# Performance work log

Measured on AMD Instinct MI355X. Metric: run time of the kernel, lower is better.

Reference implementation:

```python
import jax, jax.numpy as jnp
import numpy as np

D_MODEL = 1024
N_HEAD = 16
N_BR = 4
DH = D_MODEL // N_HEAD            # 64
H_TOT = N_BR * N_HEAD             # 64
SCALE = float(np.pi / np.sqrt(3.0))
ATTN_SCALE = DH ** -0.5


def _rope(x):
    # x: (B, H, T, Dh). Non-interleaved variant: output is cat of the two rotated halves.
    B, H, T, Dh = x.shape
    inv_freq = 1.0 / (10000.0 ** (jnp.arange(0, Dh, 2, dtype=jnp.float32) / Dh))  # (Dh/2,)
    t = jnp.arange(T, dtype=jnp.float32)
    freqs = t[:, None] * inv_freq[None, :]        # (T, Dh/2)
    cos = jnp.cos(freqs)[None, None]              # (1,1,T,Dh/2)
    sin = jnp.sin(freqs)[None, None]
    x1 = x[..., 0::2]
    x2 = x[..., 1::2]
    return jnp.concatenate([-x2 * sin + x1 * cos, x1 * sin + x2 * cos], axis=-1)


def setup_inputs() -> dict:
    key = jax.random.key(0)
    ks = jax.random.split(key, 8)
    s = 0.02
    B, T = 1, 1024
    return {
        "X": jax.random.normal(ks[0], (B, T, D_MODEL), jnp.float32),
        "Wq": jax.random.normal(ks[1], (D_MODEL, H_TOT * DH), jnp.float32) * s,
        "bq": jnp.zeros((H_TOT * DH,), jnp.float32),
        "Wk": jax.random.normal(ks[2], (D_MODEL, D_MODEL), jnp.float32) * s,
        "bk": jnp.zeros((D_MODEL,), jnp.float32),
        "Wv": jax.random.normal(ks[3], (D_MODEL, H_TOT * DH), jnp.float32) * s,
        "bv": jnp.zeros((H_TOT * DH,), jnp.float32),
        "sink_scalars": jax.random.normal(ks[4], (H_TOT, 1, 1), jnp.float32) * s,
        "v_nulls": jax.random.normal(ks[5], (H_TOT, DH), jnp.float32) * s,
        "Wo": jax.random.normal(ks[6], (D_MODEL, D_MODEL), jnp.float32) * s,
        "bo": jnp.zeros((D_MODEL,), jnp.float32),
    }


def reference(X, Wq, bq, Wk, bk, Wv, bv, sink_scalars, v_nulls, Wo, bo):
    B, T, C = X.shape
    q = (X @ Wq + bq).reshape(B, T, H_TOT, DH).transpose(0, 2, 1, 3)   # (B,H,T,Dh)
    v = (X @ Wv + bv).reshape(B, T, H_TOT, DH).transpose(0, 2, 1, 3)
    k_base = (X @ Wk + bk).reshape(B, T, N_HEAD, DH).transpose(0, 2, 1, 3)  # (B,Nh,T,Dh)
    k = jnp.tile(k_base, (1, N_BR, 1, 1))                               # (B,H,T,Dh)

    q = _rope(q)
    k = _rope(k)

    scores = jnp.einsum('bhtd,bhsd->bhts', q, k) * ATTN_SCALE           # (B,H,T,T)
    key_self = jnp.clip(jnp.sum(k * k, axis=-1), 1e-6, None)            # (B,H,T)
    denom = jnp.sqrt(key_self)[:, :, None, :]                           # (B,H,1,T)
    w = jax.nn.softplus(scores / denom)

    causal = jnp.tril(jnp.ones((T, T), dtype=bool))                     # keep lower triangle
    w = jnp.where(causal[None, None], w, 0.0)
    w = w * jax.nn.sigmoid(SCALE * w)

    sinks = jnp.tanh(sink_scalars).reshape(1, H_TOT, 1, 1) + 1e-6       # (1,H,1,1)
    alpha = 1.0 / (jnp.sum(w, axis=-1, keepdims=True) + sinks + 1e-6)   # (B,H,T,1)
    probs_tokens = w * alpha
    probs_sink = sinks * alpha                                          # (B,H,T,1)

    out_tokens = jnp.einsum('bhts,bhsd->bhtd', probs_tokens, v)
    out_sinks = probs_sink * v_nulls[None, :, None, :]                  # (B,H,T,Dh)
    context = out_tokens + out_sinks                                    # (B,H,T,Dh)

    context = context.reshape(B, N_BR, N_HEAD, T, DH)
    context = context.transpose(0, 1, 3, 2, 4).reshape(B, N_BR, T, C)
    y = context @ Wo + bo                                               # (B,N_BR,T,C)
    return jnp.mean(y, axis=1)


if __name__ == "__main__":
    out = reference(**setup_inputs())
    print(out.shape)
```

## Files before the change

### kernel.cpp

```cpp
#include <hip/hip_runtime.h>
#include <math.h>

#define SILU_SCALE 1.8137993642342178f
#define QKV_N 9216
#define LN2 0.6931471805599453f
#define DNSCALE 0.18033688011112042f

typedef __attribute__((ext_vector_type(8))) short bf16x8;
typedef __attribute__((ext_vector_type(4))) float f32x4;

#if __has_builtin(__builtin_amdgcn_exp2f)
#define EXP2(x) __builtin_amdgcn_exp2f(x)
#else
#define EXP2(x) exp2f(x)
#endif
#if __has_builtin(__builtin_amdgcn_logf)
#define LOG2(x) __builtin_amdgcn_logf(x)
#else
#define LOG2(x) __log2f(x)
#endif

__device__ __forceinline__ unsigned short f2bf(float f){
    union { float f; unsigned int i; } u; u.f = f;
    unsigned int r = u.i + 0x7FFFu + ((u.i >> 16) & 1u);
    return (unsigned short)(r >> 16);
}
__device__ __forceinline__ float bf2f(unsigned short s){
    union { unsigned int i; float f; } u; u.i = ((unsigned int)s) << 16;
    return u.f;
}
__device__ __forceinline__ unsigned int pack_bf2(float lo, float hi){
    unsigned int i0 = __float_as_uint(lo) + 0x8000u;
    unsigned int i1 = __float_as_uint(hi) + 0x8000u;
    return __builtin_amdgcn_perm(i1, i0, 0x07060302u);
}

__device__ __forceinline__ void gload_lds16(const void* g, void* l){
    __builtin_amdgcn_global_load_lds(
        (const __attribute__((address_space(1))) void*)g,
        (__attribute__((address_space(3))) void*)l, 16, 0, 0);
}

__global__ __launch_bounds__(256) void prep_kernel(
    const float* __restrict__ X,
    const float* __restrict__ Wq, const float* __restrict__ Wk,
    const float* __restrict__ Wv, const float* __restrict__ Wo,
    const float* __restrict__ bq, const float* __restrict__ bk,
    const float* __restrict__ bv,
    unsigned short* __restrict__ Xb, unsigned short* __restrict__ WqkvT,
    unsigned short* __restrict__ WoT, float* __restrict__ qkvb)
{
    __shared__ float t[64][65];
    int b = blockIdx.x;
    const int tid = threadIdx.x;

    if (b >= 2560){
        if (b < 3072){
            int i = ((b - 2560) * 256 + tid) * 8;
            float4 a = *(const float4*)&X[i];
            float4 c = *(const float4*)&X[i + 4];
            union { unsigned short u[8]; uint4 v; } o;
            o.u[0]=f2bf(a.x); o.u[1]=f2bf(a.y); o.u[2]=f2bf(a.z); o.u[3]=f2bf(a.w);
            o.u[4]=f2bf(c.x); o.u[5]=f2bf(c.y); o.u[6]=f2bf(c.z); o.u[7]=f2bf(c.w);
            *(uint4*)&Xb[i] = o.v;
        } else {
            int i = (b - 3072) * 256 + tid;
            float v;
            if (i < 4096) v = bq[i];
            else if (i < 5120) v = bk[i - 4096];
            else v = bv[i - 5120];
            qkvb[i] = v;
        }
        return;
    }

    const float* W; unsigned short* Wt; int N, tiles_x;
    if (b < 1024)      { W = Wq; Wt = WqkvT;                       N = 4096; tiles_x = 64; }
    else if (b < 1280) { b -= 1024; W = Wk; Wt = WqkvT + (size_t)4096*1024; N = 1024; tiles_x = 16; }
    else if (b < 2304) { b -= 1280; W = Wv; Wt = WqkvT + (size_t)5120*1024; N = 4096; tiles_x = 64; }
    else               { b -= 2304; W = Wo; Wt = WoT;              N = 1024; tiles_x = 16; }

    const int k0 = (b / tiles_x) * 64, n0 = (b % tiles_x) * 64;
    const int lr  = tid >> 4;
    const int lc4 = (tid & 15) * 4;
    #pragma unroll
    for (int p = 0; p < 4; p++){
        int r = lr + p * 16;
        float4 v = *(const float4*)&W[(size_t)(k0 + r) * N + n0 + lc4];
        t[lc4+0][r] = v.x; t[lc4+1][r] = v.y;
        t[lc4+2][r] = v.z; t[lc4+3][r] = v.w;
    }
    __syncthreads();
    const int wr  = tid >> 3;
    const int wc8 = (tid & 7) * 8;
    #pragma unroll
    for (int p = 0; p < 2; p++){
        int r = wr + p * 32;
        union { unsigned short u[8]; uint4 v; } o;
        #pragma unroll
        for (int j = 0; j < 8; j++) o.u[j] = f2bf(t[r][wc8 + j]);
        *(uint4*)&Wt[(size_t)(n0 + r) * 1024 + k0 + wc8] = o.v;
    }
}

template<int BM, int BN, int OUTBF>
__global__ __launch_bounds__(256) void gemm_k(
    const unsigned short* __restrict__ A,
    const unsigned short* __restrict__ Bt,
    const float* __restrict__ bias,
    void* __restrict__ Cout, int M, int N, int K)
{
    constexpr int MT = BM / 32;
    constexpr int NT = BN / 32;
    __shared__ unsigned short As[BM * 64];
    __shared__ unsigned short Bs[BN * 64];
    const int tid  = threadIdx.x;
    const int wave = tid >> 6;
    const int lane = tid & 63;
    const int l15  = lane & 15;
    const int quad = lane >> 4;
    const int m0 = blockIdx.y * BM;
    const int n0 = blockIdx.x * BN;
    const int wm = (wave >> 1) * (BM / 2);
    const int wn = (wave & 1) * (BN / 2);

    f32x4 acc[MT][NT];
    #pragma unroll
    for (int i = 0; i < MT; i++)
        #pragma unroll
        for (int j = 0; j < NT; j++)
            acc[i][j] = (f32x4){0.f, 0.f, 0.f, 0.f};

    for (int k0 = 0; k0 < K; k0 += 64){
        #pragma unroll
        for (int j = 0; j < (BM * 8) / 256; j++){
            int bslot = j * 256 + wave * 64;
            int slot = bslot + lane;
            int row = slot >> 3, phys = slot & 7;
            int c = phys ^ (row & 7);
            gload_lds16(&A[(size_t)(m0 + row) * K + k0 + c * 8], &As[bslot * 8]);
        }
        #pragma unroll
        for (int j = 0; j < (BN * 8) / 256; j++){
            int bslot = j * 256 + wave * 64;
            int slot = bslot + lane;
            int row = slot >> 3, phys = slot & 7;
            int c = phys ^ (row & 7);
            gload_lds16(&Bt[(size_t)(n0 + row) * K + k0 + c * 8], &Bs[bslot * 8]);
        }
        __syncthreads();
        #pragma unroll
        for (int ks = 0; ks < 2; ks++){
            bf16x8 af[MT], bfr[NT];
            #pragma unroll
            for (int i = 0; i < MT; i++){
                int row = wm + i * 16 + l15;
                int phys = (ks * 4 + quad) ^ (row & 7);
                af[i] = *(const bf16x8*)&As[row * 64 + phys * 8];
            }
            #pragma unroll
            for (int j = 0; j < NT; j++){
                int row = wn + j * 16 + l15;
                int phys = (ks * 4 + quad) ^ (row & 7);
                bfr[j] = *(const bf16x8*)&Bs[row * 64 + phys * 8];
            }
            #pragma unroll
            for (int i = 0; i < MT; i++)
                #pragma unroll
                for (int j = 0; j < NT; j++)
                    acc[i][j] = __builtin_amdgcn_mfma_f32_16x16x32_bf16(af[i], bfr[j], acc[i][j], 0, 0, 0);
        }
        __syncthreads();
    }
    #pragma unroll
    for (int i = 0; i < MT; i++){
        #pragma unroll
        for (int j = 0; j < NT; j++){
            int col = n0 + wn + j * 16 + l15;
            float bv = bias[col];
            #pragma unroll
            for (int r = 0; r < 4; r++){
                int row = m0 + wm + i * 16 + quad * 4 + r;
                float v = acc[i][j][r] + bv;
                if (OUTBF) ((unsigned short*)Cout)[(size_t)row * N + col] = f2bf(v);
                else       ((float*)Cout)[(size_t)row * N + col] = v;
            }
        }
    }
}

__global__ __launch_bounds__(256) void gemm_wo(
    const unsigned short* __restrict__ A,
    const unsigned short* __restrict__ Bt,
    float* __restrict__ P)
{
    constexpr int BM = 128, BN = 64, MT = 4, NT = 2;
    __shared__ unsigned short As[BM * 64];
    __shared__ unsigned short Bs[BN * 64];
    const int tid  = threadIdx.x;
    const int wave = tid >> 6;
    const int lane = tid & 63;
    const int l15  = lane & 15;
    const int quad = lane >> 4;
    const int m0 = blockIdx.y * BM;
    const int n0 = blockIdx.x * BN;
    const int kz = blockIdx.z;
    const int wm = (wave >> 1) * 64;
    const int wn = (wave & 1) * 32;

    f32x4 acc[MT][NT];
    #pragma unroll
    for (int i = 0; i < MT; i++)
        #pragma unroll
        for (int j = 0; j < NT; j++)
            acc[i][j] = (f32x4){0.f, 0.f, 0.f, 0.f};

    const int kbeg = kz * 512;
    for (int k0 = kbeg; k0 < kbeg + 512; k0 += 64){
        #pragma unroll
        for (int j = 0; j < (BM * 8) / 256; j++){
            int bslot = j * 256 + wave * 64;
            int slot = bslot + lane;
            int row = slot >> 3, phys = slot & 7;
            int c = phys ^ (row & 7);
            gload_lds16(&A[(size_t)(m0 + row) * 1024 + k0 + c * 8], &As[bslot * 8]);
        }
        #pragma unroll
        for (int j = 0; j < (BN * 8) / 256; j++){
            int bslot = j * 256 + wave * 64;
            int slot = bslot + lane;
            int row = slot >> 3, phys = slot & 7;
            int c = phys ^ (row & 7);
            gload_lds16(&Bt[(size_t)(n0 + row) * 1024 + k0 + c * 8], &Bs[bslot * 8]);
        }
        __syncthreads();
        #pragma unroll
        for (int ks = 0; ks < 2; ks++){
            bf16x8 af[MT], bfr[NT];
            #pragma unroll
            for (int i = 0; i < MT; i++){
                int row = wm + i * 16 + l15;
                int phys = (ks * 4 + quad) ^ (row & 7);
                af[i] = *(const bf16x8*)&As[row * 64 + phys * 8];
            }
            #pragma unroll
            for (int j = 0; j < NT; j++){
                int row = wn + j * 16 + l15;
                int phys = (ks * 4 + quad) ^ (row & 7);
                bfr[j] = *(const bf16x8*)&Bs[row * 64 + phys * 8];
            }
            #pragma unroll
            for (int i = 0; i < MT; i++)
                #pragma unroll
                for (int j = 0; j < NT; j++)
                    acc[i][j] = __builtin_amdgcn_mfma_f32_16x16x32_bf16(af[i], bfr[j], acc[i][j], 0, 0, 0);
        }
        __syncthreads();
    }
    float* Pz = P + (size_t)kz * 1024 * 1024;
    #pragma unroll
    for (int i = 0; i < MT; i++){
        #pragma unroll
        for (int j = 0; j < NT; j++){
            int col = n0 + wn + j * 16 + l15;
            #pragma unroll
            for (int r = 0; r < 4; r++){
                int row = m0 + wm + i * 16 + quad * 4 + r;
                Pz[(size_t)row * 1024 + col] = acc[i][j][r];
            }
        }
    }
}

__global__ void wo_reduce(const float* __restrict__ P, const float* __restrict__ bo,
                          float* __restrict__ out)
{
    int i = (blockIdx.x * 256 + threadIdx.x) * 4;
    float4 a = *(const float4*)&P[i];
    float4 b = *(const float4*)&P[1024 * 1024 + i];
    float4 c = *(const float4*)&bo[i & 1023];
    float4 o;
    o.x = a.x + b.x + c.x; o.y = a.y + b.y + c.y;
    o.z = a.z + b.z + c.z; o.w = a.w + b.w + c.w;
    *(float4*)&out[i] = o;
}

__global__ void rope_kernel(unsigned short* __restrict__ qkv, float* __restrict__ dninv)
{
    int idx = blockIdx.x * blockDim.x + threadIdx.x;
    if (idx < 65536){
        int t = idx >> 6, h = idx & 63;
        unsigned short* p = qkv + (size_t)t * QKV_N + h * 64;
        uint4 raw[8];
        #pragma unroll
        for (int i = 0; i < 8; i++) raw[i] = *(const uint4*)(p + i * 8);
        const unsigned short* rp = (const unsigned short*)raw;
        float x[64];
        #pragma unroll
        for (int i = 0; i < 64; i++) x[i] = bf2f(rp[i]);
        unsigned short o[64];
        #pragma unroll
        for (int d = 0; d < 32; d++){
            float inv = EXP2(-(float)d * 0.4152410118609203f);
            float s, c; __sincosf((float)t * inv, &s, &c);
            float x1 = x[2*d], x2 = x[2*d+1];
            o[d]      = f2bf(x1 * c - x2 * s);
            o[d + 32] = f2bf(x1 * s + x2 * c);
        }
        #pragma unroll
        for (int i = 0; i < 8; i++) *(uint4*)(p + i * 8) = ((const uint4*)o)[i];
    } else {
        idx -= 65536;
        int t = idx >> 4, h = idx & 15;
        unsigned short* p = qkv + (size_t)t * QKV_N + 4096 + h * 64;
        uint4 raw[8];
        #pragma unroll
        for (int i = 0; i < 8; i++) raw[i] = *(const uint4*)(p + i * 8);
        const unsigned short* rp = (const unsigned short*)raw;
        float x[64];
        #pragma unroll
        for (int i = 0; i < 64; i++) x[i] = bf2f(rp[i]);
        unsigned short o[64];
        float ss = 0.f;
        #pragma unroll
        for (int d = 0; d < 32; d++){
            float inv = EXP2(-(float)d * 0.4152410118609203f);
            float s, c; __sincosf((float)t * inv, &s, &c);
            float x1 = x[2*d], x2 = x[2*d+1];
            float a = x1 * c - x2 * s;
            float b = x1 * s + x2 * c;
            ss = fmaf(a, a, fmaf(b, b, ss));
            o[d]      = f2bf(a);
            o[d + 32] = f2bf(b);
        }
        #pragma unroll
        for (int i = 0; i < 8; i++) *(uint4*)(p + i * 8) = ((const uint4*)o)[i];
        dninv[h * 1024 + t] = DNSCALE * rsqrtf(fmaxf(ss, 1e-6f));
    }
}

__global__ __launch_bounds__(512) void attn_mfma(
    const unsigned short* __restrict__ qkv,
    const float* __restrict__ dninv,
    const float* __restrict__ sinks, const float* __restrict__ vnulls,
    unsigned short* __restrict__ ctx)
{
    __shared__ unsigned short ks[64 * 64];
    __shared__ unsigned short vt[64 * 64];
    __shared__ unsigned short ws[2][64][72];
    __shared__ float dl[64];
    __shared__ float dsum[8][16];

    const int tid  = threadIdx.x;
    const int wave = tid >> 6;
    const int tile = wave >> 2;
    const int w    = wave & 3;
    const int lane = tid & 63;
    const int l15  = lane & 15;
    const int quad = lane >> 4;
    const int h  = blockIdx.y;
    const int kh = h & 15;
    const int pi = blockIdx.x;
    const int qtB = 15 - pi;
    const int qt  = tile ? qtB : pi;
    const int t0  = qt << 6;

    const unsigned short* Q  = qkv;
    const unsigned short* Kp = qkv + 4096;
    const unsigned short* V  = qkv + 5120;

    bf16x8 qf0, qf1;
    {
        const unsigned short* qp = Q + (size_t)(t0 + w * 16 + l15) * QKV_N + h * 64;
        qf0 = *(const bf16x8*)(qp + quad * 8);
        qf1 = *(const bf16x8*)(qp + 32 + quad * 8);
    }

    f32x4 acc_o[4];
    #pragma unroll
    for (int i = 0; i < 4; i++) acc_o[i] = (f32x4){0.f, 0.f, 0.f, 0.f};
    float den = 0.f;
    const int q_glob = t0 + w * 16 + l15;

    const int pr  = (tid & 255) >> 3;
    const int cch = tid & 7;

    for (int st = 0; st <= qtB; st++){
        const int s0 = st << 6;
        __syncthreads();

        {
            int bslot = wave * 64;
            int slot = bslot + lane;
            int row = slot >> 3, phys = slot & 7;
            int c = phys ^ (row & 7);
            gload_lds16(&Kp[(size_t)(s0 + row) * QKV_N + kh * 64 + c * 8], &ks[bslot * 8]);
        }
        if (tid < 256){
            uint4 g0 = *(const uint4*)&V[(size_t)(s0 + 2 * pr)     * QKV_N + h * 64 + cch * 8];
            uint4 g1 = *(const uint4*)&V[(size_t)(s0 + 2 * pr + 1) * QKV_N + h * 64 + cch * 8];
            const unsigned short* p0 = (const unsigned short*)&g0;
            const unsigned short* p1 = (const unsigned short*)&g1;
            #pragma unroll
            for (int j = 0; j < 8; j++){
                int d = cch * 8 + j;
                int physc = (pr >> 2) ^ ((d ^ (d >> 3)) & 7);
                unsigned int val = (unsigned int)p0[j] | ((unsigned int)p1[j] << 16);
                ((unsigned int*)vt)[d * 32 + physc * 4 + (pr & 3)] = val;
            }
        } else if (tid < 320){
            dl[tid - 256] = dninv[kh * 1024 + s0 + (tid - 256)];
        }
        __syncthreads();

        if (st > qt) continue;
        const bool diag = (st == qt);

        #pragma unroll
        for (int nt = 0; nt < 4; nt++){
            const int sbase = nt * 16 + quad * 4;
            uint2* wp = (uint2*)&ws[tile][w * 16 + l15][sbase];
            if (diag && nt > w){ *wp = (uint2){0u, 0u}; continue; }

            f32x4 sc = (f32x4){0.f, 0.f, 0.f, 0.f};
            {
                int srow = nt * 16 + l15;
                int ph0 = quad ^ (srow & 7);
                int ph1 = (4 + quad) ^ (srow & 7);
                bf16x8 kf0 = *(const bf16x8*)&ks[srow * 64 + ph0 * 8];
                bf16x8 kf1 = *(const bf16x8*)&ks[srow * 64 + ph1 * 8];
                sc = __builtin_amdgcn_mfma_f32_16x16x32_bf16(kf0, qf0, sc, 0, 0, 0);
                sc = __builtin_amdgcn_mfma_f32_16x16x32_bf16(kf1, qf1, sc, 0, 0, 0);
            }
            float da[4];
            *(float4*)da = *(const float4*)&dl[sbase];
            float w4[4];
            #pragma unroll
            for (int r = 0; r < 4; r++){
                float y = sc[r] * da[r];
                float p = EXP2(-fabsf(y));
                float u = fmaxf(y, 0.f) + LOG2(1.f + p);
                float e3 = EXP2(-SILU_SCALE * u);
                float wv = __fdividef(LN2 * u, 1.f + e3);
                wv = (s0 + sbase + r <= q_glob) ? wv : 0.f;
                den += wv;
                w4[r] = wv;
            }
            uint2 pk;
            pk.x = pack_bf2(w4[0], w4[1]);
            pk.y = pack_bf2(w4[2], w4[3]);
            *wp = pk;
        }

        {
            const int prow = w * 16 + l15;
            bf16x8 pf0 = *(const bf16x8*)&ws[tile][prow][quad * 8];
            bf16x8 pf1 = *(const bf16x8*)&ws[tile][prow][32 + quad * 8];
            const bool skip_hi = diag && (w <= 1);
            #pragma unroll
            for (int dt = 0; dt < 4; dt++){
                int d = dt * 16 + l15;
                int swz = (d ^ (d >> 3)) & 7;
                bf16x8 vf0 = *(const bf16x8*)&vt[d * 64 + (quad ^ swz) * 8];
                acc_o[dt] = __builtin_amdgcn_mfma_f32_16x16x32_bf16(pf0, vf0, acc_o[dt], 0, 0, 0);
                if (!skip_hi){
                    bf16x8 vf1 = *(const bf16x8*)&vt[d * 64 + ((4 + quad) ^ swz) * 8];
                    acc_o[dt] = __builtin_amdgcn_mfma_f32_16x16x32_bf16(pf1, vf1, acc_o[dt], 0, 0, 0);
                }
            }
        }
    }

    den += __shfl_xor(den, 16);
    den += __shfl_xor(den, 32);
    if (quad == 0) dsum[wave][l15] = den;
    float den4[4];
    *(float4*)den4 = *(const float4*)&dsum[wave][quad * 4];

    float sinkv = tanhf(sinks[h]) + 1e-6f;
    #pragma unroll
    for (int r = 0; r < 4; r++){
        int qg = t0 + w * 16 + quad * 4 + r;
        float alpha = __fdividef(1.f, den4[r] + sinkv + 1e-6f);
        #pragma unroll
        for (int dt = 0; dt < 4; dt++){
            int d = dt * 16 + l15;
            float o = (acc_o[dt][r] + sinkv * vnulls[h * 64 + d]) * alpha;
            ctx[((size_t)h * 1024 + qg) * 64 + d] = f2bf(o);
        }
    }
}

__global__ void avg_kernel(const unsigned short* __restrict__ ctx, unsigned short* __restrict__ avg)
{
    int i8 = (blockIdx.x * 256 + threadIdx.x) * 8;
    int t = i8 >> 10, c = i8 & 1023;
    int nh = c >> 6, d = c & 63;
    float s[8] = {};
    #pragma unroll
    for (int br = 0; br < 4; br++){
        uint4 v = *(const uint4*)&ctx[((size_t)(br * 16 + nh) * 1024 + t) * 64 + d];
        const unsigned short* p = (const unsigned short*)&v;
        #pragma unroll
        for (int j = 0; j < 8; j++) s[j] += bf2f(p[j]);
    }
    union { unsigned short u[8]; uint4 v; } o;
    #pragma unroll
    for (int j = 0; j < 8; j++) o.u[j] = f2bf(0.25f * s[j]);
    *(uint4*)&avg[i8] = o.v;
}

extern "C" void kernel_launch(void* const* d_in, const int* in_sizes, int n_in,
                              void* d_out, int out_size, void* d_ws, size_t ws_size,
                              hipStream_t stream)
{
    (void)in_sizes; (void)n_in; (void)out_size; (void)ws_size;
    const float* X      = (const float*)d_in[0];
    const float* Wq     = (const float*)d_in[1];
    const float* bq     = (const float*)d_in[2];
    const float* Wk     = (const float*)d_in[3];
    const float* bk     = (const float*)d_in[4];
    const float* Wv     = (const float*)d_in[5];
    const float* bv     = (const float*)d_in[6];
    const float* sinks  = (const float*)d_in[7];
    const float* vnulls = (const float*)d_in[8];
    const float* Wo     = (const float*)d_in[9];
    const float* bo     = (const float*)d_in[10];
    float* out = (float*)d_out;

    unsigned short* w16   = (unsigned short*)d_ws;
    unsigned short* Xb    = w16;
    unsigned short* WqkvT = Xb    + (size_t)1024 * 1024;
    unsigned short* QKVb  = WqkvT + (size_t)QKV_N * 1024;
    unsigned short* WoT   = QKVb  + (size_t)1024 * QKV_N;
    unsigned short* ctxb  = WoT   + (size_t)1024 * 1024;
    unsigned short* avgb  = ctxb  + (size_t)64 * 1024 * 64;
    float* qkvb = (float*)(avgb + (size_t)1024 * 1024);
    float* dnf  = qkvb + QKV_N;
    float* pWo  = (float*)WqkvT;

    dim3 blk(256);
    prep_kernel<<<3108, blk, 0, stream>>>(X, Wq, Wk, Wv, Wo, bq, bk, bv,
                                          Xb, WqkvT, WoT, qkvb);
    gemm_k<128, 96, 1><<<dim3(96, 8), blk, 0, stream>>>(Xb, WqkvT, qkvb, QKVb, 1024, QKV_N, 1024);
    rope_kernel<<<320, blk, 0, stream>>>(QKVb, dnf);
    attn_mfma<<<dim3(8, 64), dim3(512), 0, stream>>>(QKVb, dnf, sinks, vnulls, ctxb);
    avg_kernel<<<512, blk, 0, stream>>>(ctxb, avgb);
    gemm_wo<<<dim3(16, 8, 2), blk, 0, stream>>>(avgb, WoT, pWo);
    wo_reduce<<<1024, blk, 0, stream>>>(pWo, bo, out);
}
```

Before: 209.2 us.

## Fuse Q RoPE into attention and switch to one query tile per block

RoPE for Q moves into the attention kernel: each lane rotates its own Q fragment on load, so the rope pass now touches only K and the Q read-modify-write through global memory goes away. The attention kernel also drops the paired-tile scheme (two causal tiles per 512-thread block) and uses 256-thread blocks that each handle one query tile, launched heaviest tiles first across a 64x16 grid. This spreads work over more, smaller blocks in exchange for weaker load balancing per block and some duplicated sincos work across heads.

```diff
diff --git a/kernel.cpp b/kernel.cpp
--- a/kernel.cpp
+++ b/kernel.cpp
@@ -285,61 +285,37 @@
     *(float4*)&out[i] = o;
 }
 
-__global__ void rope_kernel(unsigned short* __restrict__ qkv, float* __restrict__ dninv)
+__global__ void rope_k(unsigned short* __restrict__ qkv, float* __restrict__ dninv)
 {
     int idx = blockIdx.x * blockDim.x + threadIdx.x;
-    if (idx < 65536){
-        int t = idx >> 6, h = idx & 63;
-        unsigned short* p = qkv + (size_t)t * QKV_N + h * 64;
-        uint4 raw[8];
-        #pragma unroll
-        for (int i = 0; i < 8; i++) raw[i] = *(const uint4*)(p + i * 8);
-        const unsigned short* rp = (const unsigned short*)raw;
-        float x[64];
-        #pragma unroll
-        for (int i = 0; i < 64; i++) x[i] = bf2f(rp[i]);
-        unsigned short o[64];
-        #pragma unroll
-        for (int d = 0; d < 32; d++){
-            float inv = EXP2(-(float)d * 0.4152410118609203f);
-            float s, c; __sincosf((float)t * inv, &s, &c);
-            float x1 = x[2*d], x2 = x[2*d+1];
-            o[d]      = f2bf(x1 * c - x2 * s);
-            o[d + 32] = f2bf(x1 * s + x2 * c);
-        }
-        #pragma unroll
-        for (int i = 0; i < 8; i++) *(uint4*)(p + i * 8) = ((const uint4*)o)[i];
-    } else {
-        idx -= 65536;
-        int t = idx >> 4, h = idx & 15;
-        unsigned short* p = qkv + (size_t)t * QKV_N + 4096 + h * 64;
-        uint4 raw[8];
-        #pragma unroll
-        for (int i = 0; i < 8; i++) raw[i] = *(const uint4*)(p + i * 8);
-        const unsigned short* rp = (const unsigned short*)raw;
-        float x[64];
-        #pragma unroll
-        for (int i = 0; i < 64; i++) x[i] = bf2f(rp[i]);
-        unsigned short o[64];
-        float ss = 0.f;
-        #pragma unroll
-        for (int d = 0; d < 32; d++){
-            float inv = EXP2(-(float)d * 0.4152410118609203f);
-            float s, c; __sincosf((float)t * inv, &s, &c);
-            float x1 = x[2*d], x2 = x[2*d+1];
-            float a = x1 * c - x2 * s;
-            float b = x1 * s + x2 * c;
-            ss = fmaf(a, a, fmaf(b, b, ss));
-            o[d]      = f2bf(a);
-            o[d + 32] = f2bf(b);
-        }
-        #pragma unroll
-        for (int i = 0; i < 8; i++) *(uint4*)(p + i * 8) = ((const uint4*)o)[i];
-        dninv[h * 1024 + t] = DNSCALE * rsqrtf(fmaxf(ss, 1e-6f));
-    }
-}
-
-__global__ __launch_bounds__(512) void attn_mfma(
+    int t = idx >> 4, h = idx & 15;
+    unsigned short* p = qkv + (size_t)t * QKV_N + 4096 + h * 64;
+    uint4 raw[8];
+    #pragma unroll
+    for (int i = 0; i < 8; i++) raw[i] = *(const uint4*)(p + i * 8);
+    const unsigned short* rp = (const unsigned short*)raw;
+    float x[64];
+    #pragma unroll
+    for (int i = 0; i < 64; i++) x[i] = bf2f(rp[i]);
+    unsigned short o[64];
+    float ss = 0.f;
+    #pragma unroll
+    for (int d = 0; d < 32; d++){
+        float inv = EXP2(-(float)d * 0.4152410118609203f);
+        float s, c; __sincosf((float)t * inv, &s, &c);
+        float x1 = x[2*d], x2 = x[2*d+1];
+        float a = x1 * c - x2 * s;
+        float b = x1 * s + x2 * c;
+        ss = fmaf(a, a, fmaf(b, b, ss));
+        o[d]      = f2bf(a);
+        o[d + 32] = f2bf(b);
+    }
+    #pragma unroll
+    for (int i = 0; i < 8; i++) *(uint4*)(p + i * 8) = ((const uint4*)o)[i];
+    dninv[h * 1024 + t] = DNSCALE * rsqrtf(fmaxf(ss, 1e-6f));
+}
+
+__global__ __launch_bounds__(256) void attn_mfma(
     const unsigned short* __restrict__ qkv,
     const float* __restrict__ dninv,
     const float* __restrict__ sinks, const float* __restrict__ vnulls,
@@ -347,23 +323,19 @@
 {
     __shared__ unsigned short ks[64 * 64];
     __shared__ unsigned short vt[64 * 64];
-    __shared__ unsigned short ws[2][64][72];
+    __shared__ unsigned short ws[64][72];
     __shared__ float dl[64];
-    __shared__ float dsum[8][16];
+    __shared__ float dsum[4][16];
 
     const int tid  = threadIdx.x;
     const int wave = tid >> 6;
-    const int tile = wave >> 2;
-    const int w    = wave & 3;
     const int lane = tid & 63;
     const int l15  = lane & 15;
     const int quad = lane >> 4;
-    const int h  = blockIdx.y;
+    const int h  = blockIdx.x;
     const int kh = h & 15;
-    const int pi = blockIdx.x;
-    const int qtB = 15 - pi;
-    const int qt  = tile ? qtB : pi;
-    const int t0  = qt << 6;
+    const int qt = 15 - blockIdx.y;
+    const int t0 = qt << 6;
 
     const unsigned short* Q  = qkv;
     const unsigned short* Kp = qkv + 4096;
@@ -371,32 +343,48 @@
 
     bf16x8 qf0, qf1;
     {
-        const unsigned short* qp = Q + (size_t)(t0 + w * 16 + l15) * QKV_N + h * 64;
-        qf0 = *(const bf16x8*)(qp + quad * 8);
-        qf1 = *(const bf16x8*)(qp + 32 + quad * 8);
+        const int t = t0 + wave * 16 + l15;
+        const unsigned short* qp = Q + (size_t)t * QKV_N + h * 64 + quad * 16;
+        uint4 r0 = *(const uint4*)qp;
+        uint4 r1 = *(const uint4*)(qp + 8);
+        unsigned short e[16];
+        *(uint4*)&e[0] = r0; *(uint4*)&e[8] = r1;
+        unsigned short o0[8], o1[8];
+        #pragma unroll
+        for (int j = 0; j < 8; j++){
+            int dp = quad * 8 + j;
+            float inv = EXP2(-(float)dp * 0.4152410118609203f);
+            float s, c; __sincosf((float)t * inv, &s, &c);
+            float x1 = bf2f(e[2*j]), x2 = bf2f(e[2*j+1]);
+            o0[j] = f2bf(x1 * c - x2 * s);
+            o1[j] = f2bf(x1 * s + x2 * c);
+        }
+        qf0 = *(const bf16x8*)o0;
+        qf1 = *(const bf16x8*)o1;
     }
 
     f32x4 acc_o[4];
     #pragma unroll
     for (int i = 0; i < 4; i++) acc_o[i] = (f32x4){0.f, 0.f, 0.f, 0.f};
     float den = 0.f;
-    const int q_glob = t0 + w * 16 + l15;
-
-    const int pr  = (tid & 255) >> 3;
+    const int q_glob = t0 + wave * 16 + l15;
+
+    const int pr  = tid >> 3;
     const int cch = tid & 7;
 
-    for (int st = 0; st <= qtB; st++){
+    for (int st = 0; st <= qt; st++){
         const int s0 = st << 6;
         __syncthreads();
 
-        {
-            int bslot = wave * 64;
+        #pragma unroll
+        for (int i = 0; i < 2; i++){
+            int bslot = wave * 128 + i * 64;
             int slot = bslot + lane;
             int row = slot >> 3, phys = slot & 7;
             int c = phys ^ (row & 7);
             gload_lds16(&Kp[(size_t)(s0 + row) * QKV_N + kh * 64 + c * 8], &ks[bslot * 8]);
         }
-        if (tid < 256){
+        {
             uint4 g0 = *(const uint4*)&V[(size_t)(s0 + 2 * pr)     * QKV_N + h * 64 + cch * 8];
             uint4 g1 = *(const uint4*)&V[(size_t)(s0 + 2 * pr + 1) * QKV_N + h * 64 + cch * 8];
             const unsigned short* p0 = (const unsigned short*)&g0;
@@ -408,19 +396,17 @@
                 unsigned int val = (unsigned int)p0[j] | ((unsigned int)p1[j] << 16);
                 ((unsigned int*)vt)[d * 32 + physc * 4 + (pr & 3)] = val;
             }
-        } else if (tid < 320){
-            dl[tid - 256] = dninv[kh * 1024 + s0 + (tid - 256)];
-        }
+        }
+        if (tid < 64) dl[tid] = dninv[kh * 1024 + s0 + tid];
         __syncthreads();
 
-        if (st > qt) continue;
         const bool diag = (st == qt);
 
         #pragma unroll
         for (int nt = 0; nt < 4; nt++){
             const int sbase = nt * 16 + quad * 4;
-            uint2* wp = (uint2*)&ws[tile][w * 16 + l15][sbase];
-            if (diag && nt > w){ *wp = (uint2){0u, 0u}; continue; }
+            uint2* wp = (uint2*)&ws[wave * 16 + l15][sbase];
+            if (diag && nt > wave){ *wp = (uint2){0u, 0u}; continue; }
 
             f32x4 sc = (f32x4){0.f, 0.f, 0.f, 0.f};
             {
@@ -453,10 +439,10 @@
         }
 
         {
-            const int prow = w * 16 + l15;
-            bf16x8 pf0 = *(const bf16x8*)&ws[tile][prow][quad * 8];
-            bf16x8 pf1 = *(const bf16x8*)&ws[tile][prow][32 + quad * 8];
-            const bool skip_hi = diag && (w <= 1);
+            const int prow = wave * 16 + l15;
+            bf16x8 pf0 = *(const bf16x8*)&ws[prow][quad * 8];
+            bf16x8 pf1 = *(const bf16x8*)&ws[prow][32 + quad * 8];
+            const bool skip_hi = diag && (wave <= 1);
             #pragma unroll
             for (int dt = 0; dt < 4; dt++){
                 int d = dt * 16 + l15;
@@ -480,7 +466,7 @@
     float sinkv = tanhf(sinks[h]) + 1e-6f;
     #pragma unroll
     for (int r = 0; r < 4; r++){
-        int qg = t0 + w * 16 + quad * 4 + r;
+        int qg = t0 + wave * 16 + quad * 4 + r;
         float alpha = __fdividef(1.f, den4[r] + sinkv + 1e-6f);
         #pragma unroll
         for (int dt = 0; dt < 4; dt++){
@@ -543,8 +529,8 @@
     prep_kernel<<<3108, blk, 0, stream>>>(X, Wq, Wk, Wv, Wo, bq, bk, bv,
                                           Xb, WqkvT, WoT, qkvb);
     gemm_k<128, 96, 1><<<dim3(96, 8), blk, 0, stream>>>(Xb, WqkvT, qkvb, QKVb, 1024, QKV_N, 1024);
-    rope_kernel<<<320, blk, 0, stream>>>(QKVb, dnf);
-    attn_mfma<<<dim3(8, 64), dim3(512), 0, stream>>>(QKVb, dnf, sinks, vnulls, ctxb);
+    rope_k<<<64, blk, 0, stream>>>(QKVb, dnf);
+    attn_mfma<<<dim3(64, 16), blk, 0, stream>>>(QKVb, dnf, sinks, vnulls, ctxb);
     avg_kernel<<<512, blk, 0, stream>>>(ctxb, avgb);
     gemm_wo<<<dim3(16, 8, 2), blk, 0, stream>>>(avgb, WoT, pWo);
     wo_reduce<<<1024, blk, 0, stream>>>(pWo, bo, out);
```

After: 201.4 us. 3.7% less time.
